# Kernel optimization log

Measured on AMD Instinct MI355X. Metric: run time of the kernel, lower is better.

Reference implementation:

```python
import jax, jax.numpy as jnp
import numpy as np

VOCAB = 50000
B, T, D_OUT = 32, 512, 256
E_DIMS = (300, 300, 200)


def setup_inputs() -> dict:
    key = jax.random.key(0)
    ks = jax.random.split(key, 8)
    ids = jax.random.randint(ks[0], (B, T), 0, VOCAB)
    E0 = jax.random.normal(ks[1], (VOCAB, E_DIMS[0]), dtype=jnp.float32)
    E1 = jax.random.normal(ks[2], (VOCAB, E_DIMS[1]), dtype=jnp.float32)
    E2 = jax.random.normal(ks[3], (VOCAB, E_DIMS[2]), dtype=jnp.float32)
    # Glorot-ish scaled projection weights
    W0 = jax.random.normal(ks[4], (E_DIMS[0], D_OUT), dtype=jnp.float32) / np.sqrt(E_DIMS[0])
    W1 = jax.random.normal(ks[5], (E_DIMS[1], D_OUT), dtype=jnp.float32) / np.sqrt(E_DIMS[1])
    W2 = jax.random.normal(ks[6], (E_DIMS[2], D_OUT), dtype=jnp.float32) / np.sqrt(E_DIMS[2])
    Wa = jax.random.normal(ks[7], (D_OUT, 1), dtype=jnp.float32) / np.sqrt(D_OUT)
    return {
        "ids": ids,
        "E0": E0, "E1": E1, "E2": E2,
        "W0": W0, "b0": jnp.zeros((D_OUT,), jnp.float32),
        "W1": W1, "b1": jnp.zeros((D_OUT,), jnp.float32),
        "W2": W2, "b2": jnp.zeros((D_OUT,), jnp.float32),
        "Wa": Wa, "ba": jnp.zeros((1,), jnp.float32),
    }


def reference(ids, E0, E1, E2, W0, b0, W1, b1, W2, b2, Wa, ba):
    # Per-source embedding gather + Dense projection -> [B, T, D_OUT]
    p0 = E0[ids] @ W0 + b0
    p1 = E1[ids] @ W1 + b1
    p2 = E2[ids] @ W2 + b2
    projected = jnp.stack([p0, p1, p2], axis=2)  # [B, T, n_emb, D]
    # Attention Dense(1) over D, softmax over the n_emb axis
    logits = jnp.einsum('btnd,do->btno', projected, Wa) + ba  # [B, T, n, 1]
    alphas = jax.nn.softmax(logits, axis=2)
    # Weighted combine: matmul(projected^T, alphas) then squeeze -> [B, T, D]
    out = jnp.einsum('btnd,btn->btd', projected, alphas[..., 0])
    return out
```

## Files before the change

### kernel.cpp

```cpp
#include <hip/hip_runtime.h>
#include <hip/hip_bf16.h>

typedef __attribute__((ext_vector_type(8))) short short8;
typedef __attribute__((ext_vector_type(4))) float floatx4;
typedef unsigned short ushort_t;
typedef unsigned int uint_t;

#define DOUT   256
#define KPAD   864
#define XPITCH 904
#define TB     16
#define NTOK   16384
#define NPREP_T 27
#define NPREP_U 225

static __device__ inline uint_t pack2bf(float x, float y) {
    __hip_bfloat162 h = __float22bfloat162_rn(make_float2(x, y));
    return *(uint_t*)&h;
}

__global__ __launch_bounds__(256) void k_prep(
    const float* __restrict__ W0, const float* __restrict__ W1,
    const float* __restrict__ W2,
    const float* __restrict__ b0, const float* __restrict__ b1,
    const float* __restrict__ b2,
    const float* __restrict__ Wa, const float* __restrict__ ba,
    float* __restrict__ u, float* __restrict__ lb, ushort_t* __restrict__ Wt)
{
    __shared__ ushort_t tile[32][256];
    int tid = threadIdx.x;
    if (blockIdx.x < NPREP_T) {
        int k0 = blockIdx.x * 32;
        for (int idx = tid; idx < 32 * 256; idx += 256) {
            int kk = idx >> 8, d = idx & 255;
            int kp = k0 + kk;
            float v = 0.f;
            const float* src = nullptr;
            if (kp < 320)      { if (kp < 300) src = W0 + kp * DOUT; }
            else if (kp < 640) { int o = kp - 320; if (o < 300) src = W1 + o * DOUT; }
            else               { int o = kp - 640; if (o < 200) src = W2 + o * DOUT; }
            if (src) v = src[d];
            tile[kk][d] = (ushort_t)(pack2bf(v, 0.f) & 0xFFFFu);
        }
        __syncthreads();
        int d = tid;
        #pragma unroll
        for (int g = 0; g < 4; ++g) {
            union { uint4 v; ushort_t s[8]; } p;
            #pragma unroll
            for (int j = 0; j < 8; ++j) p.s[j] = tile[g * 8 + j][d];
            *(uint4*)(Wt + (size_t)d * KPAD + k0 + g * 8) = p.v;
        }
    } else {
        int lane = tid & 63;
        int w = tid >> 6;
        int kp = (blockIdx.x - NPREP_T) * 4 + w;
        if (kp > 898) return;
        const float* row = nullptr;
        if (kp < 320)       { if (kp < 300) row = W0 + kp * DOUT; }
        else if (kp < 640)  { int o = kp - 320; if (o < 300) row = W1 + o * DOUT; }
        else if (kp < 864)  { int o = kp - 640; if (o < 200) row = W2 + o * DOUT; }
        else if (kp >= 896) { int n = kp - 896; row = (n == 0) ? b0 : ((n == 1) ? b1 : b2); }
        float acc = 0.f;
        if (row) {
            #pragma unroll
            for (int j = lane; j < DOUT; j += 64)
                acc += row[j] * Wa[j];
        }
        for (int off = 32; off > 0; off >>= 1) acc += __shfl_down(acc, off);
        if (lane == 0) {
            if (kp < 896) u[kp] = acc;
            else          lb[kp - 896] = acc + ba[0];
        }
    }
}

#define MFMA_STEP(ACC, KC) {                                                   \
    short8 a0 = *(const short8*)&Xs[mrow][(KC) + kg8];                         \
    _Pragma("unroll")                                                          \
    for (int nt = 0; nt < 4; ++nt) {                                           \
        short8 bv = *(const short8*)(bp[nt] + (KC));                           \
        ACC[nt] = __builtin_amdgcn_mfma_f32_16x16x32_bf16(a0, bv, ACC[nt], 0, 0, 0); \
    }                                                                          \
}

__global__ __launch_bounds__(256, 5) void k_main(
    const int* __restrict__ ids,
    const float* __restrict__ E0, const float* __restrict__ E1,
    const float* __restrict__ E2,
    const float* __restrict__ b0, const float* __restrict__ b1,
    const float* __restrict__ b2,
    const float* __restrict__ u, const float* __restrict__ lb,
    const ushort_t* __restrict__ Wt,
    float* __restrict__ out)
{
    __shared__ __align__(16) ushort_t Xs[TB][XPITCH];
    __shared__ float alphaS[TB][4];

    int tid = threadIdx.x;
    int tok0 = blockIdx.x * TB;

    int trow = tid >> 4, sub = tid & 15;
    int id = ids[tok0 + trow];
    uint2* Xd2 = (uint2*)&Xs[trow][0];
    const float4* E0v = (const float4*)E0;
    const float4* E1v = (const float4*)E1;
    const float4* E2v = (const float4*)E2;
    float4 f4z = make_float4(0.f, 0.f, 0.f, 0.f);

    float4 g[14];
    {
        const float4* p0 = E0v + (size_t)id * 75;
        const float4* p1 = E1v + (size_t)id * 75;
        const float4* p2 = E2v + (size_t)id * 50;
        g[0] = p0[sub];      g[1] = p0[sub + 16];
        g[2] = p0[sub + 32]; g[3] = p0[sub + 48];
        g[4] = (sub < 11) ? p0[sub + 64] : f4z;
        g[5] = p1[sub];      g[6] = p1[sub + 16];
        g[7] = p1[sub + 32]; g[8] = p1[sub + 48];
        g[9] = (sub < 11) ? p1[sub + 64] : f4z;
        g[10] = p2[sub];      g[11] = p2[sub + 16];
        g[12] = p2[sub + 32];
        g[13] = (sub < 2) ? p2[sub + 48] : f4z;
    }

    float l0 = 0.f, l1 = 0.f, l2 = 0.f;
    #pragma unroll
    for (int j = 0; j < 5; ++j) {
        int i = sub + 16 * j;
        float4 t = g[j];
        float4 uu = *(const float4*)(u + 4 * i);
        l0 += t.x * uu.x + t.y * uu.y + t.z * uu.z + t.w * uu.w;
        Xd2[i] = make_uint2(pack2bf(t.x, t.y), pack2bf(t.z, t.w));
    }
    #pragma unroll
    for (int j = 0; j < 5; ++j) {
        int i = sub + 16 * j;
        float4 t = g[5 + j];
        float4 uu = *(const float4*)(u + 320 + 4 * i);
        l1 += t.x * uu.x + t.y * uu.y + t.z * uu.z + t.w * uu.w;
        Xd2[80 + i] = make_uint2(pack2bf(t.x, t.y), pack2bf(t.z, t.w));
    }
    #pragma unroll
    for (int j = 0; j < 4; ++j) {
        int i = sub + 16 * j;
        float4 t = g[10 + j];
        float4 uu = *(const float4*)(u + 640 + 4 * i);
        l2 += t.x * uu.x + t.y * uu.y + t.z * uu.z + t.w * uu.w;
        Xd2[160 + i] = make_uint2(pack2bf(t.x, t.y), pack2bf(t.z, t.w));
    }

    #pragma unroll
    for (int off = 8; off > 0; off >>= 1) {
        l0 += __shfl_down(l0, off);
        l1 += __shfl_down(l1, off);
        l2 += __shfl_down(l2, off);
    }
    if (sub == 0) {
        l0 += lb[0]; l1 += lb[1]; l2 += lb[2];
        float m = fmaxf(l0, fmaxf(l1, l2));
        float e0 = __expf(l0 - m), e1 = __expf(l1 - m), e2 = __expf(l2 - m);
        float inv = 1.f / (e0 + e1 + e2);
        alphaS[trow][0] = e0 * inv;
        alphaS[trow][1] = e1 * inv;
        alphaS[trow][2] = e2 * inv;
    }
    __syncthreads();

    int lane = tid & 63;
    int w = tid >> 6;
    int mrow = lane & 15;
    int kg8 = (lane >> 4) * 8;

    const ushort_t* bp[4];
    #pragma unroll
    for (int nt = 0; nt < 4; ++nt)
        bp[nt] = Wt + (size_t)(w * 64 + nt * 16 + mrow) * KPAD + kg8;

    floatx4 acc0[4], acc1[4], acc2[4];
    #pragma unroll
    for (int nt = 0; nt < 4; ++nt) {
        floatx4 z = {0.f, 0.f, 0.f, 0.f};
        acc0[nt] = z; acc1[nt] = z; acc2[nt] = z;
    }

    #pragma unroll
    for (int kc = 0; kc < 320; kc += 32)   MFMA_STEP(acc0, kc);
    #pragma unroll
    for (int kc = 320; kc < 640; kc += 32) MFMA_STEP(acc1, kc);
    #pragma unroll
    for (int kc = 640; kc < 864; kc += 32) MFMA_STEP(acc2, kc);

    float bb0[4], bb1[4], bb2[4];
    #pragma unroll
    for (int nt = 0; nt < 4; ++nt) {
        int n = w * 64 + nt * 16 + mrow;
        bb0[nt] = b0[n];
        bb1[nt] = b1[n];
        bb2[nt] = b2[n];
    }
    #pragma unroll
    for (int r = 0; r < 4; ++r) {
        int tok = (lane >> 4) * 4 + r;
        float a0 = alphaS[tok][0], a1 = alphaS[tok][1], a2 = alphaS[tok][2];
        size_t rowoff = (size_t)(tok0 + tok) * DOUT;
        #pragma unroll
        for (int nt = 0; nt < 4; ++nt) {
            int n = w * 64 + nt * 16 + mrow;
            float v = a0 * (acc0[nt][r] + bb0[nt])
                    + a1 * (acc1[nt][r] + bb1[nt])
                    + a2 * (acc2[nt][r] + bb2[nt]);
            out[rowoff + n] = v;
        }
    }
}

extern "C" void kernel_launch(void* const* d_in, const int* in_sizes, int n_in,
                              void* d_out, int out_size, void* d_ws, size_t ws_size,
                              hipStream_t stream) {
    const int*   ids = (const int*)d_in[0];
    const float* E0  = (const float*)d_in[1];
    const float* E1  = (const float*)d_in[2];
    const float* E2  = (const float*)d_in[3];
    const float* W0  = (const float*)d_in[4];
    const float* b0  = (const float*)d_in[5];
    const float* W1  = (const float*)d_in[6];
    const float* b1  = (const float*)d_in[7];
    const float* W2  = (const float*)d_in[8];
    const float* b2  = (const float*)d_in[9];
    const float* Wa  = (const float*)d_in[10];
    const float* ba  = (const float*)d_in[11];

    float* u     = (float*)d_ws;
    float* lb    = u + 896;
    ushort_t* Wt = (ushort_t*)((char*)d_ws + 4096);

    k_prep<<<NPREP_T + NPREP_U, 256, 0, stream>>>(W0, W1, W2, b0, b1, b2, Wa, ba,
                                                  u, lb, Wt);
    k_main<<<NTOK / TB, 256, 0, stream>>>(ids, E0, E1, E2, b0, b1, b2, u, lb, Wt,
                                          (float*)d_out);
}
```

Measured before the change: 213.3 us.

## Pre-scale embeddings by alpha and fuse three projections into one K=864 GEMM

Applies the softmax weights to each embedding row before the bf16 conversion, so the three projections collapse into a single K=864 accumulation instead of three separate accumulator sets. Tokens per block grow from 16 to 32 with 512 threads, and each wave now computes a 2x2 tile of 16x16 MFMA blocks. The weights are pre-swizzled into a fragment-major layout so each lane loads contiguous 16-byte chunks, and padding columns are zeroed explicitly. This reduces accumulator registers and improves reuse of the weight fragments, at the cost of extra bf16 rounding from scaling before quantization and a larger shared-memory footprint per block.

```diff
diff --git a/kernel.cpp b/kernel.cpp
--- a/kernel.cpp
+++ b/kernel.cpp
@@ -8,8 +8,8 @@
 
 #define DOUT   256
 #define KPAD   864
-#define XPITCH 904
-#define TB     16
+#define XPITCH 872
+#define TB     32
 #define NTOK   16384
 #define NPREP_T 27
 #define NPREP_U 225
@@ -17,6 +17,11 @@
 static __device__ inline uint_t pack2bf(float x, float y) {
     __hip_bfloat162 h = __float22bfloat162_rn(make_float2(x, y));
     return *(uint_t*)&h;
+}
+static __device__ inline ushort_t f2bf(float f) {
+    union { float f; uint_t u; } a; a.f = f;
+    uint_t u = a.u;
+    return (ushort_t)((u + 0x7FFFu + ((u >> 16) & 1u)) >> 16);
 }
 
 __global__ __launch_bounds__(256) void k_prep(
@@ -25,31 +30,38 @@
     const float* __restrict__ b0, const float* __restrict__ b1,
     const float* __restrict__ b2,
     const float* __restrict__ Wa, const float* __restrict__ ba,
-    float* __restrict__ u, float* __restrict__ lb, ushort_t* __restrict__ Wt)
+    float* __restrict__ u, float* __restrict__ lb, ushort_t* __restrict__ Wtf)
 {
-    __shared__ ushort_t tile[32][256];
+    __shared__ ushort_t tile[32][258];
     int tid = threadIdx.x;
     if (blockIdx.x < NPREP_T) {
-        int k0 = blockIdx.x * 32;
-        for (int idx = tid; idx < 32 * 256; idx += 256) {
-            int kk = idx >> 8, d = idx & 255;
-            int kp = k0 + kk;
-            float v = 0.f;
+        int kc = blockIdx.x;
+        for (int idx = tid; idx < 32 * 64; idx += 256) {
+            int kk = idx >> 6, c4 = idx & 63;
+            int kp = kc * 32 + kk;
+            float4 v = make_float4(0.f, 0.f, 0.f, 0.f);
             const float* src = nullptr;
             if (kp < 320)      { if (kp < 300) src = W0 + kp * DOUT; }
             else if (kp < 640) { int o = kp - 320; if (o < 300) src = W1 + o * DOUT; }
             else               { int o = kp - 640; if (o < 200) src = W2 + o * DOUT; }
-            if (src) v = src[d];
-            tile[kk][d] = (ushort_t)(pack2bf(v, 0.f) & 0xFFFFu);
+            if (src) v = *(const float4*)(src + 4 * c4);
+            tile[kk][4 * c4 + 0] = f2bf(v.x);
+            tile[kk][4 * c4 + 1] = f2bf(v.y);
+            tile[kk][4 * c4 + 2] = f2bf(v.z);
+            tile[kk][4 * c4 + 3] = f2bf(v.w);
         }
         __syncthreads();
-        int d = tid;
+        int lane = tid & 63;
+        int ntg = tid >> 6;
+        int kq = (lane >> 4) * 8;
+        int nc = lane & 15;
         #pragma unroll
-        for (int g = 0; g < 4; ++g) {
+        for (int i = 0; i < 4; ++i) {
+            int nt = ntg * 4 + i;
             union { uint4 v; ushort_t s[8]; } p;
             #pragma unroll
-            for (int j = 0; j < 8; ++j) p.s[j] = tile[g * 8 + j][d];
-            *(uint4*)(Wt + (size_t)d * KPAD + k0 + g * 8) = p.v;
+            for (int j = 0; j < 8; ++j) p.s[j] = tile[kq + j][nt * 16 + nc];
+            *(uint4*)(Wtf + ((size_t)(nt * 27 + kc) * 64 + lane) * 8) = p.v;
         }
     } else {
         int lane = tid & 63;
@@ -75,23 +87,14 @@
     }
 }
 
-#define MFMA_STEP(ACC, KC) {                                                   \
-    short8 a0 = *(const short8*)&Xs[mrow][(KC) + kg8];                         \
-    _Pragma("unroll")                                                          \
-    for (int nt = 0; nt < 4; ++nt) {                                           \
-        short8 bv = *(const short8*)(bp[nt] + (KC));                           \
-        ACC[nt] = __builtin_amdgcn_mfma_f32_16x16x32_bf16(a0, bv, ACC[nt], 0, 0, 0); \
-    }                                                                          \
-}
-
-__global__ __launch_bounds__(256, 5) void k_main(
+__global__ __launch_bounds__(512, 4) void k_main(
     const int* __restrict__ ids,
     const float* __restrict__ E0, const float* __restrict__ E1,
     const float* __restrict__ E2,
     const float* __restrict__ b0, const float* __restrict__ b1,
     const float* __restrict__ b2,
     const float* __restrict__ u, const float* __restrict__ lb,
-    const ushort_t* __restrict__ Wt,
+    const ushort_t* __restrict__ Wtf,
     float* __restrict__ out)
 {
     __shared__ __align__(16) ushort_t Xs[TB][XPITCH];
@@ -103,68 +106,75 @@
     int trow = tid >> 4, sub = tid & 15;
     int id = ids[tok0 + trow];
     uint2* Xd2 = (uint2*)&Xs[trow][0];
-    const float4* E0v = (const float4*)E0;
-    const float4* E1v = (const float4*)E1;
-    const float4* E2v = (const float4*)E2;
+    const float4* p0 = (const float4*)E0 + (size_t)id * 75;
+    const float4* p1 = (const float4*)E1 + (size_t)id * 75;
+    const float4* p2 = (const float4*)E2 + (size_t)id * 50;
     float4 f4z = make_float4(0.f, 0.f, 0.f, 0.f);
 
     float4 g[14];
-    {
-        const float4* p0 = E0v + (size_t)id * 75;
-        const float4* p1 = E1v + (size_t)id * 75;
-        const float4* p2 = E2v + (size_t)id * 50;
-        g[0] = p0[sub];      g[1] = p0[sub + 16];
-        g[2] = p0[sub + 32]; g[3] = p0[sub + 48];
-        g[4] = (sub < 11) ? p0[sub + 64] : f4z;
-        g[5] = p1[sub];      g[6] = p1[sub + 16];
-        g[7] = p1[sub + 32]; g[8] = p1[sub + 48];
-        g[9] = (sub < 11) ? p1[sub + 64] : f4z;
-        g[10] = p2[sub];      g[11] = p2[sub + 16];
-        g[12] = p2[sub + 32];
-        g[13] = (sub < 2) ? p2[sub + 48] : f4z;
-    }
+    g[0] = p0[sub];      g[1] = p0[sub + 16];
+    g[2] = p0[sub + 32]; g[3] = p0[sub + 48];
+    g[4] = (sub < 11) ? p0[sub + 64] : f4z;
+    g[5] = p1[sub];      g[6] = p1[sub + 16];
+    g[7] = p1[sub + 32]; g[8] = p1[sub + 48];
+    g[9] = (sub < 11) ? p1[sub + 64] : f4z;
+    g[10] = p2[sub];      g[11] = p2[sub + 16];
+    g[12] = p2[sub + 32];
+    g[13] = (sub < 2) ? p2[sub + 48] : f4z;
+    __builtin_amdgcn_sched_barrier(0);
 
     float l0 = 0.f, l1 = 0.f, l2 = 0.f;
     #pragma unroll
     for (int j = 0; j < 5; ++j) {
-        int i = sub + 16 * j;
+        float4 t = g[j], uu = *(const float4*)(u + 4 * (sub + 16 * j));
+        l0 += t.x * uu.x + t.y * uu.y + t.z * uu.z + t.w * uu.w;
+    }
+    #pragma unroll
+    for (int j = 0; j < 5; ++j) {
+        float4 t = g[5 + j], uu = *(const float4*)(u + 320 + 4 * (sub + 16 * j));
+        l1 += t.x * uu.x + t.y * uu.y + t.z * uu.z + t.w * uu.w;
+    }
+    #pragma unroll
+    for (int j = 0; j < 4; ++j) {
+        float4 t = g[10 + j], uu = *(const float4*)(u + 640 + 4 * (sub + 16 * j));
+        l2 += t.x * uu.x + t.y * uu.y + t.z * uu.z + t.w * uu.w;
+    }
+    #pragma unroll
+    for (int m = 1; m < 16; m <<= 1) {
+        l0 += __shfl_xor(l0, m);
+        l1 += __shfl_xor(l1, m);
+        l2 += __shfl_xor(l2, m);
+    }
+    l0 += lb[0]; l1 += lb[1]; l2 += lb[2];
+    float mx = fmaxf(l0, fmaxf(l1, l2));
+    float e0 = __expf(l0 - mx), e1 = __expf(l1 - mx), e2 = __expf(l2 - mx);
+    float inv = 1.f / (e0 + e1 + e2);
+    float a0 = e0 * inv, a1 = e1 * inv, a2 = e2 * inv;
+    if (sub == 0) { alphaS[trow][0] = a0; alphaS[trow][1] = a1; alphaS[trow][2] = a2; }
+
+    #pragma unroll
+    for (int j = 0; j < 5; ++j) {
         float4 t = g[j];
-        float4 uu = *(const float4*)(u + 4 * i);
-        l0 += t.x * uu.x + t.y * uu.y + t.z * uu.z + t.w * uu.w;
-        Xd2[i] = make_uint2(pack2bf(t.x, t.y), pack2bf(t.z, t.w));
-    }
-    #pragma unroll
-    for (int j = 0; j < 5; ++j) {
-        int i = sub + 16 * j;
+        Xd2[sub + 16 * j] = make_uint2(pack2bf(a0 * t.x, a0 * t.y), pack2bf(a0 * t.z, a0 * t.w));
+    }
+    #pragma unroll
+    for (int j = 0; j < 5; ++j) {
         float4 t = g[5 + j];
-        float4 uu = *(const float4*)(u + 320 + 4 * i);
-        l1 += t.x * uu.x + t.y * uu.y + t.z * uu.z + t.w * uu.w;
-        Xd2[80 + i] = make_uint2(pack2bf(t.x, t.y), pack2bf(t.z, t.w));
-    }
-    #pragma unroll
-    for (int j = 0; j < 4; ++j) {
-        int i = sub + 16 * j;
+        Xd2[80 + sub + 16 * j] = make_uint2(pack2bf(a1 * t.x, a1 * t.y), pack2bf(a1 * t.z, a1 * t.w));
+    }
+    #pragma unroll
+    for (int j = 0; j < 3; ++j) {
         float4 t = g[10 + j];
-        float4 uu = *(const float4*)(u + 640 + 4 * i);
-        l2 += t.x * uu.x + t.y * uu.y + t.z * uu.z + t.w * uu.w;
-        Xd2[160 + i] = make_uint2(pack2bf(t.x, t.y), pack2bf(t.z, t.w));
-    }
-
-    #pragma unroll
-    for (int off = 8; off > 0; off >>= 1) {
-        l0 += __shfl_down(l0, off);
-        l1 += __shfl_down(l1, off);
-        l2 += __shfl_down(l2, off);
-    }
-    if (sub == 0) {
-        l0 += lb[0]; l1 += lb[1]; l2 += lb[2];
-        float m = fmaxf(l0, fmaxf(l1, l2));
-        float e0 = __expf(l0 - m), e1 = __expf(l1 - m), e2 = __expf(l2 - m);
-        float inv = 1.f / (e0 + e1 + e2);
-        alphaS[trow][0] = e0 * inv;
-        alphaS[trow][1] = e1 * inv;
-        alphaS[trow][2] = e2 * inv;
-    }
+        Xd2[160 + sub + 16 * j] = make_uint2(pack2bf(a2 * t.x, a2 * t.y), pack2bf(a2 * t.z, a2 * t.w));
+    }
+    if (sub < 2) {
+        float4 t = g[13];
+        Xd2[160 + 48 + sub] = make_uint2(pack2bf(a2 * t.x, a2 * t.y), pack2bf(a2 * t.z, a2 * t.w));
+    }
+    uint2 z2 = make_uint2(0u, 0u);
+    for (int i = 75 + sub;  i < 80;  i += 16) Xd2[i] = z2;
+    for (int i = 155 + sub; i < 160; i += 16) Xd2[i] = z2;
+    for (int i = 210 + sub; i < 218; i += 16) Xd2[i] = z2;
     __syncthreads();
 
     int lane = tid & 63;
@@ -172,45 +182,45 @@
     int mrow = lane & 15;
     int kg8 = (lane >> 4) * 8;
 
-    const ushort_t* bp[4];
-    #pragma unroll
-    for (int nt = 0; nt < 4; ++nt)
-        bp[nt] = Wt + (size_t)(w * 64 + nt * 16 + mrow) * KPAD + kg8;
-
-    floatx4 acc0[4], acc1[4], acc2[4];
-    #pragma unroll
-    for (int nt = 0; nt < 4; ++nt) {
+    const ushort_t* bq0 = Wtf + ((size_t)((2 * w + 0) * 27) * 64 + lane) * 8;
+    const ushort_t* bq1 = Wtf + ((size_t)((2 * w + 1) * 27) * 64 + lane) * 8;
+
+    floatx4 acc[2][2];
+    {
         floatx4 z = {0.f, 0.f, 0.f, 0.f};
-        acc0[nt] = z; acc1[nt] = z; acc2[nt] = z;
-    }
-
-    #pragma unroll
-    for (int kc = 0; kc < 320; kc += 32)   MFMA_STEP(acc0, kc);
-    #pragma unroll
-    for (int kc = 320; kc < 640; kc += 32) MFMA_STEP(acc1, kc);
-    #pragma unroll
-    for (int kc = 640; kc < 864; kc += 32) MFMA_STEP(acc2, kc);
-
-    float bb0[4], bb1[4], bb2[4];
-    #pragma unroll
-    for (int nt = 0; nt < 4; ++nt) {
-        int n = w * 64 + nt * 16 + mrow;
-        bb0[nt] = b0[n];
-        bb1[nt] = b1[n];
-        bb2[nt] = b2[n];
-    }
-    #pragma unroll
-    for (int r = 0; r < 4; ++r) {
-        int tok = (lane >> 4) * 4 + r;
-        float a0 = alphaS[tok][0], a1 = alphaS[tok][1], a2 = alphaS[tok][2];
-        size_t rowoff = (size_t)(tok0 + tok) * DOUT;
+        acc[0][0] = z; acc[0][1] = z; acc[1][0] = z; acc[1][1] = z;
+    }
+
+    #pragma unroll
+    for (int kc = 0; kc < 27; ++kc) {
+        short8 av0 = *(const short8*)&Xs[mrow][kc * 32 + kg8];
+        short8 av1 = *(const short8*)&Xs[16 + mrow][kc * 32 + kg8];
+        short8 bv0 = *(const short8*)(bq0 + kc * 512);
+        short8 bv1 = *(const short8*)(bq1 + kc * 512);
+        acc[0][0] = __builtin_amdgcn_mfma_f32_16x16x32_bf16(av0, bv0, acc[0][0], 0, 0, 0);
+        acc[1][0] = __builtin_amdgcn_mfma_f32_16x16x32_bf16(av1, bv0, acc[1][0], 0, 0, 0);
+        acc[0][1] = __builtin_amdgcn_mfma_f32_16x16x32_bf16(av0, bv1, acc[0][1], 0, 0, 0);
+        acc[1][1] = __builtin_amdgcn_mfma_f32_16x16x32_bf16(av1, bv1, acc[1][1], 0, 0, 0);
+    }
+
+    float bb0[2], bb1[2], bb2[2];
+    #pragma unroll
+    for (int nt = 0; nt < 2; ++nt) {
+        int n = (2 * w + nt) * 16 + mrow;
+        bb0[nt] = b0[n]; bb1[nt] = b1[n]; bb2[nt] = b2[n];
+    }
+    #pragma unroll
+    for (int mt = 0; mt < 2; ++mt) {
         #pragma unroll
-        for (int nt = 0; nt < 4; ++nt) {
-            int n = w * 64 + nt * 16 + mrow;
-            float v = a0 * (acc0[nt][r] + bb0[nt])
-                    + a1 * (acc1[nt][r] + bb1[nt])
-                    + a2 * (acc2[nt][r] + bb2[nt]);
-            out[rowoff + n] = v;
+        for (int r = 0; r < 4; ++r) {
+            int tok = mt * 16 + (lane >> 4) * 4 + r;
+            float t0 = alphaS[tok][0], t1 = alphaS[tok][1], t2 = alphaS[tok][2];
+            size_t rowoff = (size_t)(tok0 + tok) * DOUT;
+            #pragma unroll
+            for (int nt = 0; nt < 2; ++nt) {
+                int n = (2 * w + nt) * 16 + mrow;
+                out[rowoff + n] = acc[mt][nt][r] + t0 * bb0[nt] + t1 * bb1[nt] + t2 * bb2[nt];
+            }
         }
     }
 }
@@ -231,12 +241,12 @@
     const float* Wa  = (const float*)d_in[10];
     const float* ba  = (const float*)d_in[11];
 
-    float* u     = (float*)d_ws;
-    float* lb    = u + 896;
-    ushort_t* Wt = (ushort_t*)((char*)d_ws + 4096);
+    float* u      = (float*)d_ws;
+    float* lb     = u + 896;
+    ushort_t* Wtf = (ushort_t*)((char*)d_ws + 4096);
 
     k_prep<<<NPREP_T + NPREP_U, 256, 0, stream>>>(W0, W1, W2, b0, b1, b2, Wa, ba,
-                                                  u, lb, Wt);
-    k_main<<<NTOK / TB, 256, 0, stream>>>(ids, E0, E1, E2, b0, b1, b2, u, lb, Wt,
+                                                  u, lb, Wtf);
+    k_main<<<NTOK / TB, 512, 0, stream>>>(ids, E0, E1, E2, b0, b1, b2, u, lb, Wtf,
                                           (float*)d_out);
 }
```

Result: faster. 191.2 us (-10.3%).
